# Kernel optimization log

Measured on AMD Instinct MI355X. Metric: run time of the kernel, lower is better.

## Reference

```python
import math
import jax, jax.numpy as jnp
import numpy as np

EMBED_DIM = 1024
NUM_HEADS = 16
HEAD_DIM = EMBED_DIM // NUM_HEADS
NUM_BUCKETS = 32
MAX_DISTANCE = 128


def _relative_position_bucket(relative_position, num_buckets=NUM_BUCKETS, max_distance=MAX_DISTANCE):
    # Bidirectional T5 bucketing (matches torch reference exactly).
    num_buckets = num_buckets // 2
    relative_buckets = (relative_position > 0).astype(jnp.int32) * num_buckets
    relative_position = jnp.abs(relative_position)
    max_exact = num_buckets // 2
    is_small = relative_position < max_exact
    rp_large = jnp.log(relative_position.astype(jnp.float32) / max_exact) / math.log(max_distance / max_exact)
    rp_large = max_exact + (rp_large * (num_buckets - max_exact)).astype(jnp.int32)
    rp_large = jnp.minimum(rp_large, num_buckets - 1)
    relative_buckets = relative_buckets + jnp.where(is_small, relative_position, rp_large)
    return relative_buckets


def compute_bias(rel_emb, query_length, key_length):
    context_position = jnp.arange(query_length, dtype=jnp.int32)[:, None]
    memory_position = jnp.arange(key_length, dtype=jnp.int32)[None, :]
    relative_position = memory_position - context_position  # [q, k]
    buckets = _relative_position_bucket(relative_position)
    values = rel_emb[buckets]                 # [q, k, h]
    return jnp.transpose(values, (2, 0, 1))[None]  # [1, h, q, k]


def setup_inputs() -> dict:
    key = jax.random.key(0)
    k1, k2, k3, k4 = jax.random.split(key, 4)
    B, S = 2, 2048
    hidden_states = jax.random.normal(k1, (B, S, EMBED_DIM), dtype=jnp.float32)
    scale = 1.0 / math.sqrt(EMBED_DIM)
    W_qkv = jax.random.normal(k2, (EMBED_DIM, 3 * EMBED_DIM), dtype=jnp.float32) * scale
    W_out = jax.random.normal(k3, (EMBED_DIM, EMBED_DIM), dtype=jnp.float32) * scale
    rel_emb = jax.random.normal(k4, (NUM_BUCKETS, NUM_HEADS), dtype=jnp.float32) * 0.02
    return {"hidden_states": hidden_states, "W_qkv": W_qkv, "W_out": W_out, "rel_emb": rel_emb}


def reference(hidden_states, W_qkv, W_out, rel_emb):
    B, S, _ = hidden_states.shape
    qkv = hidden_states @ W_qkv                                # [B, S, 3*D]
    qkv = qkv.reshape(B, S, 3, NUM_HEADS, HEAD_DIM)
    qkv = jnp.transpose(qkv, (0, 3, 2, 1, 4))                  # [B, H, 3, S, dh]
    q, k, v = qkv[:, :, 0], qkv[:, :, 1], qkv[:, :, 2]
    scores = jnp.einsum('bhqd,bhkd->bhqk', q, k)               # no 1/sqrt(d) scaling (T5 style)
    scores = scores + compute_bias(rel_emb, S, S)
    attn = jax.nn.softmax(scores.astype(jnp.float32), axis=-1).astype(scores.dtype)
    out = jnp.einsum('bhqk,bhkd->bhqd', attn, v)               # [B, H, S, dh]
    out = jnp.transpose(out, (0, 2, 1, 3)).reshape(B, S, EMBED_DIM)
    return out @ W_out
```

## Files before the change

### kernel.cpp

```cpp
#include <hip/hip_runtime.h>
#include <hip/hip_bf16.h>
#include <math.h>

typedef _Float16 f16;
typedef __attribute__((ext_vector_type(8))) _Float16 f16x8;
typedef __attribute__((ext_vector_type(4))) _Float16 f16x4;
typedef __attribute__((ext_vector_type(4))) float f32x4;

#define EMBED 1024
#define NHEADS 16
#define HDIM 64
#define BATCH 2
#define SEQ 2048
#define BS 4096
#define LOG2E 1.4426950408889634f


__device__ __forceinline__ f32x4 mfma16x32(f16x8 a, f16x8 b, f32x4 c) {
  return __builtin_amdgcn_mfma_f32_16x16x32_f16(a, b, c, 0, 0, 0);
}
__device__ __forceinline__ f32x4 mfma16x16(f16x4 a, f16x4 b, f32x4 c) {
  return __builtin_amdgcn_mfma_f32_16x16x16f16(a, b, c, 0, 0, 0);
}

__global__ void cast_x_kernel(const float* __restrict__ src, f16* __restrict__ dst) {
  int i = (blockIdx.x * 256 + threadIdx.x) * 4;
  float4 v = *(const float4*)(src + i);
  f16x4 o = { (f16)v.x, (f16)v.y, (f16)v.z, (f16)v.w };
  *(f16x4*)(dst + i) = o;
}

__global__ void transpose_cast_kernel(const float* __restrict__ in, f16* __restrict__ out,
                                      int K, int N) {
  __shared__ float tile[32][33];
  int n0 = blockIdx.x * 32, k0 = blockIdx.y * 32;
  int tx = threadIdx.x & 31, ty = threadIdx.x >> 5;
#pragma unroll
  for (int r = ty; r < 32; r += 8) tile[r][tx] = in[(size_t)(k0 + r) * N + n0 + tx];
  __syncthreads();
#pragma unroll
  for (int r = ty; r < 32; r += 8) out[(size_t)(n0 + r) * K + k0 + tx] = (f16)tile[tx][r];
}

__global__ void bias_table_kernel(const float* __restrict__ rel_emb, float* __restrict__ btab) {
  int idx = blockIdx.x * 256 + threadIdx.x;
  if (idx >= 4095) return;
  int rp = idx - 2047;
  int rb = rp > 0 ? 16 : 0;
  int arp = rp < 0 ? -rp : rp;
  int loc;
  if (arp < 8) {
    loc = arp;
  } else {
    float lr = logf((float)arp * 0.125f) * (1.0f / 2.7725887222397811f);
    int t = 8 + (int)(lr * 8.0f);
    loc = t < 15 ? t : 15;
  }
  int bucket = rb + loc;
#pragma unroll
  for (int h = 0; h < 16; h++) btab[h * 4095 + idx] = rel_emb[bucket * 16 + h] * LOG2E;
}

__device__ __forceinline__ void gemm_core(const f16* __restrict__ A, const f16* __restrict__ Bt,
                                          int m0, int n0, int Kdim, f32x4 (&acc)[4][4]) {
  __shared__ __align__(16) f16 As[128 * 40];
  __shared__ __align__(16) f16 Bs[128 * 40];

  int tid = threadIdx.x;
  int lane = tid & 63, wave = tid >> 6;
  int l15 = lane & 15, quad = lane >> 4;
  int wr = (wave >> 1) * 64, wc = (wave & 1) * 64;

#pragma unroll
  for (int i = 0; i < 4; i++)
#pragma unroll
    for (int j = 0; j < 4; j++) acc[i][j] = f32x4{0.f, 0.f, 0.f, 0.f};

  for (int kt = 0; kt < Kdim / 32; kt++) {
    int kk = kt * 32;
#pragma unroll
    for (int c = 0; c < 2; c++) {
      int i = c * 256 + tid;
      int row = i >> 2, cc = (i & 3) * 8;
      int4 av = *(const int4*)(A + (size_t)(m0 + row) * Kdim + kk + cc);
      int4 bv = *(const int4*)(Bt + (size_t)(n0 + row) * Kdim + kk + cc);
      *(int4*)(&As[row * 40 + cc]) = av;
      *(int4*)(&Bs[row * 40 + cc]) = bv;
    }
    __syncthreads();
    f16x8 af[4], bf[4];
#pragma unroll
    for (int i = 0; i < 4; i++) af[i] = *(const f16x8*)(&As[(wr + i * 16 + l15) * 40 + quad * 8]);
#pragma unroll
    for (int j = 0; j < 4; j++) bf[j] = *(const f16x8*)(&Bs[(wc + j * 16 + l15) * 40 + quad * 8]);
#pragma unroll
    for (int i = 0; i < 4; i++)
#pragma unroll
      for (int j = 0; j < 4; j++) acc[i][j] = mfma16x32(af[i], bf[j], acc[i][j]);
    __syncthreads();
  }
}

__global__ __launch_bounds__(256, 2) void gemm_qkv_kernel(
    const f16* __restrict__ Xh, const f16* __restrict__ Wt,
    f16* __restrict__ Q, f16* __restrict__ K_, f16* __restrict__ Vp) {
  f32x4 acc[4][4];
  int m0 = blockIdx.y * 128, n0 = blockIdx.x * 128;
  gemm_core(Xh, Wt, m0, n0, 1024, acc);

  int lane = threadIdx.x & 63, wave = threadIdx.x >> 6;
  int l15 = lane & 15, quad = lane >> 4;
  int wr = (wave >> 1) * 64, wc = (wave & 1) * 64;
  int nq = n0 + wc;
  int which = nq >> 10;
  int h = (nq >> 6) & 15;
  int b = m0 >> 11;

  if (which == 2) {
    int s0 = (m0 & 2047) + wr;
    f16* vbase = Vp + (size_t)(b * 16 + h) * 131072 + (size_t)(s0 >> 6) * 4096;
#pragma unroll
    for (int i = 0; i < 4; i++) {
#pragma unroll
      for (int j = 0; j < 4; j++) {
        f16x4 pk = { (f16)acc[i][j][0], (f16)acc[i][j][1], (f16)acc[i][j][2], (f16)acc[i][j][3] };
        *(f16x4*)(vbase + (i * 4 + j) * 256 + lane * 4) = pk;
      }
    }
  } else {
    f16* base = (which == 0) ? Q : K_;
    float sc = (which == 0) ? LOG2E : 1.0f;
#pragma unroll
    for (int i = 0; i < 4; i++) {
#pragma unroll
      for (int j = 0; j < 4; j++) {
        int d = j * 16 + l15;
#pragma unroll
        for (int r = 0; r < 4; r++) {
          int m = m0 + wr + i * 16 + quad * 4 + r;
          int s = m & 2047;
          base[(((size_t)(b * 16 + h) * 2048 + s) << 6) + d] = (f16)(acc[i][j][r] * sc);
        }
      }
    }
  }
}

__global__ void repack_k_kernel(const f16* __restrict__ Kw, f16* __restrict__ Kp) {
  int o = blockIdx.x * 256 + threadIdx.x;
  int lane = o & 63;
  int ct = (o >> 6) & 7;
  int kt = (o >> 9) & 31;
  int bh = o >> 14;
  int c = ct >> 1, t = ct & 1;
  int l15 = lane & 15, quad = lane >> 4;
  int s = kt * 64 + c * 16 + l15;
  f16x8 v = *(const f16x8*)(Kw + ((size_t)(bh * 2048 + s) << 6) + t * 32 + quad * 8);
  *(f16x8*)(Kp + (size_t)o * 8) = v;
}

__global__ __launch_bounds__(256, 4) void attn_kernel(
    const f16* __restrict__ Q, const f16* __restrict__ Kp, const f16* __restrict__ Vp,
    const float* __restrict__ btab, f16* __restrict__ O) {
  __shared__ float bias_lds[2112];

  int qt = blockIdx.x, bh = blockIdx.y;
  int qbase = qt * 64;
  int h = bh & 15, b = bh >> 4;
  int tid = threadIdx.x, lane = tid & 63, wave = tid >> 6;
  int l15 = lane & 15, quad = lane >> 4;

  const float* brow = btab + h * 4095 + (1984 - qbase);
  for (int i = tid; i < 2111; i += 256) bias_lds[i] = brow[i];

  const f16* qptr = Q + ((size_t)bh * 2048 + qbase + wave * 16 + l15) * 64 + quad * 8;
  f16x8 qf0 = *(const f16x8*)(qptr);
  f16x8 qf1 = *(const f16x8*)(qptr + 32);

  f32x4 accO[4] = {};
  float m_i = -INFINITY, l_i = 0.f;

  const f16* kpp = Kp + (size_t)bh * 131072;
  const f16* vpp = Vp + (size_t)bh * 131072;
  const int bofs = quad * 4 - wave * 16 - l15 + 63;

  __syncthreads();

  for (int kt = 0; kt < 32; kt++) {
    const f16* kptr = kpp + kt * 4096;
    const f16* vptr = vpp + kt * 4096;
    int kb = kt * 64;
    f32x4 scT[4];
#pragma unroll
    for (int c = 0; c < 4; c++) {
      int bi = kb + c * 16 + bofs;
      scT[c] = f32x4{ bias_lds[bi], bias_lds[bi + 1], bias_lds[bi + 2], bias_lds[bi + 3] };
      f16x8 kf0 = *(const f16x8*)(kptr + (c * 2 + 0) * 512 + lane * 8);
      f16x8 kf1 = *(const f16x8*)(kptr + (c * 2 + 1) * 512 + lane * 8);
      scT[c] = mfma16x32(kf0, qf0, scT[c]);
      scT[c] = mfma16x32(kf1, qf1, scT[c]);
    }
    f16x4 vf[4][4];
#pragma unroll
    for (int c = 0; c < 4; c++)
#pragma unroll
      for (int dblk = 0; dblk < 4; dblk++)
        vf[c][dblk] = *(const f16x4*)(vptr + (c * 4 + dblk) * 256 + lane * 4);
    float mx = m_i;
#pragma unroll
    for (int c = 0; c < 4; c++)
#pragma unroll
      for (int r = 0; r < 4; r++) mx = fmaxf(mx, scT[c][r]);
    mx = fmaxf(mx, __shfl_xor(mx, 16));
    mx = fmaxf(mx, __shfl_xor(mx, 32));
    float alpha = exp2f(m_i - mx);
    m_i = mx;
    float rs = 0.f;
    f16x4 p[4];
#pragma unroll
    for (int c = 0; c < 4; c++) {
#pragma unroll
      for (int r = 0; r < 4; r++) {
        float e = exp2f(scT[c][r] - mx);
        rs += e;
        p[c][r] = (f16)e;
      }
    }
    rs += __shfl_xor(rs, 16);
    rs += __shfl_xor(rs, 32);
    l_i = l_i * alpha + rs;
    float arow[4];
#pragma unroll
    for (int r = 0; r < 4; r++) arow[r] = __shfl(alpha, quad * 4 + r);
#pragma unroll
    for (int d = 0; d < 4; d++)
#pragma unroll
      for (int r = 0; r < 4; r++) accO[d][r] *= arow[r];
#pragma unroll
    for (int c = 0; c < 4; c++)
#pragma unroll
      for (int dblk = 0; dblk < 4; dblk++)
        accO[dblk] = mfma16x16(p[c], vf[c][dblk], accO[dblk]);
  }

  float linv = 1.0f / l_i;
  float lrow[4];
#pragma unroll
  for (int r = 0; r < 4; r++) lrow[r] = __shfl(linv, quad * 4 + r);
#pragma unroll
  for (int dblk = 0; dblk < 4; dblk++) {
#pragma unroll
    for (int r = 0; r < 4; r++) {
      int q = qbase + wave * 16 + quad * 4 + r;
      O[((size_t)(b * 2048 + q) << 10) + h * 64 + dblk * 16 + l15] = (f16)(accO[dblk][r] * lrow[r]);
    }
  }
}

__global__ __launch_bounds__(256, 2) void gemm_out_kernel(
    const f16* __restrict__ Oh, const f16* __restrict__ Wt, float* __restrict__ out) {
  f32x4 acc[4][4];
  int m0 = blockIdx.y * 128, n0 = blockIdx.x * 128;
  gemm_core(Oh, Wt, m0, n0, 1024, acc);

  int lane = threadIdx.x & 63, wave = threadIdx.x >> 6;
  int l15 = lane & 15, quad = lane >> 4;
  int wr = (wave >> 1) * 64, wc = (wave & 1) * 64;
#pragma unroll
  for (int i = 0; i < 4; i++) {
#pragma unroll
    for (int j = 0; j < 4; j++) {
      int n = n0 + wc + j * 16 + l15;
#pragma unroll
      for (int r = 0; r < 4; r++) {
        int m = m0 + wr + i * 16 + quad * 4 + r;
        out[((size_t)m << 10) + n] = acc[i][j][r];
      }
    }
  }
}

extern "C" void kernel_launch(void* const* d_in, const int* in_sizes, int n_in,
                              void* d_out, int out_size, void* d_ws, size_t ws_size,
                              hipStream_t stream) {
  const float* X = (const float*)d_in[0];
  const float* Wqkv = (const float*)d_in[1];
  const float* Wout = (const float*)d_in[2];
  const float* rel = (const float*)d_in[3];

  char* ws = (char*)d_ws;
  f16* Xh     = (f16*)(ws + 0);
  f16* Kp     = (f16*)(ws + 0);
  f16* Wqkv_t = (f16*)(ws + 8388608);
  f16* Wout_t = (f16*)(ws + 14680064);
  f16* Qw     = (f16*)(ws + 16777216);
  f16* Kw     = (f16*)(ws + 25165824);
  f16* Vp     = (f16*)(ws + 33554432);
  f16* Ow     = (f16*)(ws + 41943040);
  float* btab = (float*)(ws + 50331648);

  cast_x_kernel<<<4096, 256, 0, stream>>>(X, Xh);
  transpose_cast_kernel<<<dim3(96, 32), 256, 0, stream>>>(Wqkv, Wqkv_t, 1024, 3072);
  transpose_cast_kernel<<<dim3(32, 32), 256, 0, stream>>>(Wout, Wout_t, 1024, 1024);
  bias_table_kernel<<<16, 256, 0, stream>>>(rel, btab);
  gemm_qkv_kernel<<<dim3(24, 32), 256, 0, stream>>>(Xh, Wqkv_t, Qw, Kw, Vp);
  repack_k_kernel<<<2048, 256, 0, stream>>>(Kw, Kp);
  attn_kernel<<<dim3(32, 32), 256, 0, stream>>>(Qw, Kp, Vp, btab, Ow);
  gemm_out_kernel<<<dim3(8, 32), 256, 0, stream>>>(Ow, Wout_t, (float*)d_out);
}
```

Measured before the change: 256.1 us.

## Use direct global-to-LDS loads in GEMM and widen attention V/bias loads

The GEMM core now stages A and B tiles with global_load_lds straight into unpadded LDS, skipping the round trip through registers. The V repack and the attention V fetch move from 8-byte to 16-byte vectors. Bias is kept in four shifted LDS copies so each lane reads an aligned float4, and the max and sum reductions become trees. The unpadded LDS layout may add bank conflicts on the fragment reads, and the four bias copies use more LDS per block.

```diff
diff --git a/kernel.cpp b/kernel.cpp
--- a/kernel.cpp
+++ b/kernel.cpp
@@ -21,6 +21,11 @@
 }
 __device__ __forceinline__ f32x4 mfma16x16(f16x4 a, f16x4 b, f32x4 c) {
   return __builtin_amdgcn_mfma_f32_16x16x16f16(a, b, c, 0, 0, 0);
+}
+__device__ __forceinline__ void gload_lds16(const f16* __restrict__ g, f16* l) {
+  __builtin_amdgcn_global_load_lds(
+      (const __attribute__((address_space(1))) void*)g,
+      (__attribute__((address_space(3))) void*)l, 16, 0, 0);
 }
 
 __global__ void cast_x_kernel(const float* __restrict__ src, f16* __restrict__ dst) {
@@ -63,13 +68,15 @@
 
 __device__ __forceinline__ void gemm_core(const f16* __restrict__ A, const f16* __restrict__ Bt,
                                           int m0, int n0, int Kdim, f32x4 (&acc)[4][4]) {
-  __shared__ __align__(16) f16 As[128 * 40];
-  __shared__ __align__(16) f16 Bs[128 * 40];
+  __shared__ __align__(16) f16 As[128 * 32];
+  __shared__ __align__(16) f16 Bs[128 * 32];
 
   int tid = threadIdx.x;
   int lane = tid & 63, wave = tid >> 6;
   int l15 = lane & 15, quad = lane >> 4;
   int wr = (wave >> 1) * 64, wc = (wave & 1) * 64;
+  int rowl = lane >> 2;
+  int col8 = (lane & 3) * 8;
 
 #pragma unroll
   for (int i = 0; i < 4; i++)
@@ -80,19 +87,16 @@
     int kk = kt * 32;
 #pragma unroll
     for (int c = 0; c < 2; c++) {
-      int i = c * 256 + tid;
-      int row = i >> 2, cc = (i & 3) * 8;
-      int4 av = *(const int4*)(A + (size_t)(m0 + row) * Kdim + kk + cc);
-      int4 bv = *(const int4*)(Bt + (size_t)(n0 + row) * Kdim + kk + cc);
-      *(int4*)(&As[row * 40 + cc]) = av;
-      *(int4*)(&Bs[row * 40 + cc]) = bv;
+      int row = wave * 32 + c * 16 + rowl;
+      gload_lds16(A + (size_t)(m0 + row) * Kdim + kk + col8, &As[(wave * 32 + c * 16) * 32]);
+      gload_lds16(Bt + (size_t)(n0 + row) * Kdim + kk + col8, &Bs[(wave * 32 + c * 16) * 32]);
     }
     __syncthreads();
     f16x8 af[4], bf[4];
 #pragma unroll
-    for (int i = 0; i < 4; i++) af[i] = *(const f16x8*)(&As[(wr + i * 16 + l15) * 40 + quad * 8]);
-#pragma unroll
-    for (int j = 0; j < 4; j++) bf[j] = *(const f16x8*)(&Bs[(wc + j * 16 + l15) * 40 + quad * 8]);
+    for (int i = 0; i < 4; i++) af[i] = *(const f16x8*)(&As[(wr + i * 16 + l15) * 32 + quad * 8]);
+#pragma unroll
+    for (int j = 0; j < 4; j++) bf[j] = *(const f16x8*)(&Bs[(wc + j * 16 + l15) * 32 + quad * 8]);
 #pragma unroll
     for (int i = 0; i < 4; i++)
 #pragma unroll
@@ -122,9 +126,12 @@
 #pragma unroll
     for (int i = 0; i < 4; i++) {
 #pragma unroll
-      for (int j = 0; j < 4; j++) {
-        f16x4 pk = { (f16)acc[i][j][0], (f16)acc[i][j][1], (f16)acc[i][j][2], (f16)acc[i][j][3] };
-        *(f16x4*)(vbase + (i * 4 + j) * 256 + lane * 4) = pk;
+      for (int jp = 0; jp < 2; jp++) {
+        f16x8 pk = { (f16)acc[i][2 * jp][0],     (f16)acc[i][2 * jp][1],
+                     (f16)acc[i][2 * jp][2],     (f16)acc[i][2 * jp][3],
+                     (f16)acc[i][2 * jp + 1][0], (f16)acc[i][2 * jp + 1][1],
+                     (f16)acc[i][2 * jp + 1][2], (f16)acc[i][2 * jp + 1][3] };
+        *(f16x8*)(vbase + (i * 2 + jp) * 512 + lane * 8) = pk;
       }
     }
   } else {
@@ -162,7 +169,7 @@
 __global__ __launch_bounds__(256, 4) void attn_kernel(
     const f16* __restrict__ Q, const f16* __restrict__ Kp, const f16* __restrict__ Vp,
     const float* __restrict__ btab, f16* __restrict__ O) {
-  __shared__ float bias_lds[2112];
+  __shared__ __align__(16) float bias4[4][2116];
 
   int qt = blockIdx.x, bh = blockIdx.y;
   int qbase = qt * 64;
@@ -171,7 +178,12 @@
   int l15 = lane & 15, quad = lane >> 4;
 
   const float* brow = btab + h * 4095 + (1984 - qbase);
-  for (int i = tid; i < 2111; i += 256) bias_lds[i] = brow[i];
+#pragma unroll
+  for (int j = 0; j < 4; j++)
+    for (int i = tid; i < 2116; i += 256) {
+      int src = i + j;
+      bias4[j][i] = (src <= 2110) ? brow[src] : 0.f;
+    }
 
   const f16* qptr = Q + ((size_t)bh * 2048 + qbase + wave * 16 + l15) * 64 + quad * 8;
   f16x8 qf0 = *(const f16x8*)(qptr);
@@ -194,38 +206,40 @@
 #pragma unroll
     for (int c = 0; c < 4; c++) {
       int bi = kb + c * 16 + bofs;
-      scT[c] = f32x4{ bias_lds[bi], bias_lds[bi + 1], bias_lds[bi + 2], bias_lds[bi + 3] };
+      int bj = bi & 3;
+      scT[c] = *(const f32x4*)(&bias4[bj][bi - bj]);
       f16x8 kf0 = *(const f16x8*)(kptr + (c * 2 + 0) * 512 + lane * 8);
       f16x8 kf1 = *(const f16x8*)(kptr + (c * 2 + 1) * 512 + lane * 8);
       scT[c] = mfma16x32(kf0, qf0, scT[c]);
       scT[c] = mfma16x32(kf1, qf1, scT[c]);
     }
-    f16x4 vf[4][4];
+    f16x8 vf8[4][2];
 #pragma unroll
     for (int c = 0; c < 4; c++)
 #pragma unroll
-      for (int dblk = 0; dblk < 4; dblk++)
-        vf[c][dblk] = *(const f16x4*)(vptr + (c * 4 + dblk) * 256 + lane * 4);
-    float mx = m_i;
+      for (int jp = 0; jp < 2; jp++)
+        vf8[c][jp] = *(const f16x8*)(vptr + (c * 2 + jp) * 512 + lane * 8);
+    float mc[4];
 #pragma unroll
     for (int c = 0; c < 4; c++)
-#pragma unroll
-      for (int r = 0; r < 4; r++) mx = fmaxf(mx, scT[c][r]);
+      mc[c] = fmaxf(fmaxf(scT[c][0], scT[c][1]), fmaxf(scT[c][2], scT[c][3]));
+    float mx = fmaxf(fmaxf(fmaxf(mc[0], mc[1]), fmaxf(mc[2], mc[3])), m_i);
     mx = fmaxf(mx, __shfl_xor(mx, 16));
     mx = fmaxf(mx, __shfl_xor(mx, 32));
     float alpha = exp2f(m_i - mx);
     m_i = mx;
-    float rs = 0.f;
     f16x4 p[4];
+    float rc[4];
 #pragma unroll
     for (int c = 0; c < 4; c++) {
-#pragma unroll
-      for (int r = 0; r < 4; r++) {
-        float e = exp2f(scT[c][r] - mx);
-        rs += e;
-        p[c][r] = (f16)e;
-      }
-    }
+      float e0 = exp2f(scT[c][0] - mx);
+      float e1 = exp2f(scT[c][1] - mx);
+      float e2 = exp2f(scT[c][2] - mx);
+      float e3 = exp2f(scT[c][3] - mx);
+      rc[c] = (e0 + e1) + (e2 + e3);
+      p[c][0] = (f16)e0; p[c][1] = (f16)e1; p[c][2] = (f16)e2; p[c][3] = (f16)e3;
+    }
+    float rs = (rc[0] + rc[1]) + (rc[2] + rc[3]);
     rs += __shfl_xor(rs, 16);
     rs += __shfl_xor(rs, 32);
     l_i = l_i * alpha + rs;
@@ -237,10 +251,15 @@
 #pragma unroll
       for (int r = 0; r < 4; r++) accO[d][r] *= arow[r];
 #pragma unroll
-    for (int c = 0; c < 4; c++)
-#pragma unroll
-      for (int dblk = 0; dblk < 4; dblk++)
-        accO[dblk] = mfma16x16(p[c], vf[c][dblk], accO[dblk]);
+    for (int c = 0; c < 4; c++) {
+#pragma unroll
+      for (int jp = 0; jp < 2; jp++) {
+        f16x4 vlo = __builtin_shufflevector(vf8[c][jp], vf8[c][jp], 0, 1, 2, 3);
+        f16x4 vhi = __builtin_shufflevector(vf8[c][jp], vf8[c][jp], 4, 5, 6, 7);
+        accO[2 * jp]     = mfma16x16(p[c], vlo, accO[2 * jp]);
+        accO[2 * jp + 1] = mfma16x16(p[c], vhi, accO[2 * jp + 1]);
+      }
+    }
   }
 
   float linv = 1.0f / l_i;
```

Result: faster. 234.3 us (-8.5%).
